# Kernel optimization log

Measured on AMD Instinct MI355X. Metric: run time of the kernel, lower is better.

The kernel has to match this reference:

```python
import jax, jax.numpy as jnp
import numpy as np

E = 256  # embed_dim == input_chn (required by ln_ff broadcast)
B = 256
LAMBDA_INIT = float(0.8 - 0.6 * np.exp(-0.3 * 1.0))  # layer_index = 1


def rmsnorm(x, scale, d, eps=1e-8):
    # matches torch RMSNorm: rms = ||x||_2 / sqrt(d); x / (rms + eps) * scale
    norm = jnp.linalg.norm(x, axis=-1, keepdims=True)
    rms = norm * (d ** -0.5)
    return scale * (x / (rms + eps))


def setup_inputs() -> dict:
    key = jax.random.key(0)
    ks = jax.random.split(key, 12)
    x = jax.random.normal(ks[0], (B, E, E), jnp.float32)
    s = 0.02
    return {
        "x": x,
        "Wq": jax.random.normal(ks[1], (E, 2 * E), jnp.float32) * s,
        "bq": jnp.zeros((2 * E,), jnp.float32),
        "Wk": jax.random.normal(ks[2], (E, 2 * E), jnp.float32) * s,
        "bk": jnp.zeros((2 * E,), jnp.float32),
        "Wv": jax.random.normal(ks[3], (E, E), jnp.float32) * s,
        "bv": jnp.zeros((E,), jnp.float32),
        "lq1": jax.random.normal(ks[4], (E,), jnp.float32) * 0.1,
        "lk1": jax.random.normal(ks[5], (E,), jnp.float32) * 0.1,
        "lq2": jax.random.normal(ks[6], (E,), jnp.float32) * 0.1,
        "lk2": jax.random.normal(ks[7], (E,), jnp.float32) * 0.1,
        "ln_attn_scale": jnp.ones((E,), jnp.float32),
        "norm_scale": jnp.ones((E,), jnp.float32),
        "ln_ff_scale": jnp.ones((E,), jnp.float32),
        "W1": jax.random.normal(ks[8], (E, 4 * E), jnp.float32) * s,
        "b1": jnp.zeros((4 * E,), jnp.float32),
        "W2": jax.random.normal(ks[9], (4 * E, E), jnp.float32) * s,
        "b2": jnp.zeros((E,), jnp.float32),
    }


def reference(x, Wq, bq, Wk, bk, Wv, bv, lq1, lk1, lq2, lk2,
              ln_attn_scale, norm_scale, ln_ff_scale, W1, b1, W2, b2):
    scale = E ** -0.25
    # a = ln_attn(x^T)^T  (normalize over seq dim which equals E)
    a = jnp.swapaxes(rmsnorm(jnp.swapaxes(x, -1, -2), ln_attn_scale, E), -1, -2)
    # decompose: moving average kernel=5, stride=1, edge-replicate padding 2 on seq dim
    ap = jnp.pad(a, ((0, 0), (2, 2), (0, 0)), mode="edge")
    trend = (ap[:, 0:-4] + ap[:, 1:-3] + ap[:, 2:-2] + ap[:, 3:-1] + ap[:, 4:]) / 5.0
    seasonal = a - trend
    # Q from trend, K from seasonal, V from a; all projected along the seq(=E) dim
    q = jnp.swapaxes(trend, -1, -2) @ Wq + bq          # [B, C, 2E]
    q1, q2 = jnp.split(q, 2, axis=-1)
    k = jnp.swapaxes(seasonal, -1, -2) @ Wk + bk       # [B, C, 2E]
    k1, k2 = jnp.split(k, 2, axis=-1)
    v = jnp.swapaxes(a, -1, -2) @ Wv + bv              # [B, C, E]
    a1 = jnp.einsum("bce,bde->bcd", q1, k1) * scale    # [B, C, C]
    a2 = jnp.einsum("bce,bde->bcd", q2, k2) * scale
    lam = jnp.exp(jnp.sum(lq1 * lk1)) - jnp.exp(jnp.sum(lq2 * lk2)) + LAMBDA_INIT
    d = jax.nn.softmax(a1, axis=-1) - lam * jax.nn.softmax(a2, axis=-1)
    attn = rmsnorm(d @ v, norm_scale, E) * (1.0 - LAMBDA_INIT)  # [B, C, E]
    x = x + jnp.swapaxes(attn, -1, -2)
    # FFN branch: ln_ff over last dim (chn == E), then project along seq dim
    h = jnp.swapaxes(rmsnorm(x, ln_ff_scale, E), -1, -2)        # [B, C, E]
    h = jax.nn.silu(h @ W1 + b1) @ W2 + b2                      # [B, C, E]
    x = x + jnp.swapaxes(h, -1, -2)
    return x
```

## Files before the change

### kernel.cpp

```cpp
#include <hip/hip_runtime.h>
#include <math.h>

static constexpr int E = 256;
static constexpr int BTOT = 256;

typedef __bf16 bf16;
typedef __bf16 bf16x8 __attribute__((ext_vector_type(8)));
typedef __bf16 bf16x4 __attribute__((ext_vector_type(4)));
typedef float f32x4 __attribute__((ext_vector_type(4)));

__device__ __forceinline__ void gload16(const void* g, void* l) {
  __builtin_amdgcn_global_load_lds(
      (const __attribute__((address_space(1))) void*)g,
      (__attribute__((address_space(3))) void*)l, 16, 0, 0);
}

__device__ __forceinline__ void xcd_decode(int b, int NX, int nPanels, int& x, int& g) {
  if ((nPanels & 7) == 0) {
    int gLo = b & 7;
    int t2 = b >> 3;
    x = t2 % NX;
    g = (t2 / NX) * 8 + gLo;
  } else {
    x = b % NX;
    g = b / NX;
  }
}

__device__ __forceinline__ float fsig(float x) {
  return __fdividef(1.0f, 1.0f + __expf(-x));
}

__global__ __launch_bounds__(256) void k_wT(const float* __restrict__ src,
                                            bf16* __restrict__ dst, int R, int C) {
  __shared__ float lds[32][33];
  int tiles_c = C >> 5;
  int tc = blockIdx.x % tiles_c;
  int tr = blockIdx.x / tiles_c;
  int r0 = tr << 5, c0 = tc << 5;
  int t = threadIdx.x, cc = t & 31, rr0 = t >> 5;
#pragma unroll
  for (int p = 0; p < 4; ++p) {
    int rr = rr0 + p * 8;
    lds[rr][cc] = src[(size_t)(r0 + rr) * C + (c0 + cc)];
  }
  __syncthreads();
#pragma unroll
  for (int p = 0; p < 4; ++p) {
    int rr = rr0 + p * 8;
    dst[(size_t)(c0 + rr) * R + (r0 + cc)] = (bf16)lds[cc][rr];
  }
}

__global__ void k_lam(const float* lq1, const float* lk1, const float* lq2,
                      const float* lk2, float lambda_init, float* lamOut) {
  int t = threadIdx.x;
  float v1 = lq1[t] * lk1[t];
  float v2 = lq2[t] * lk2[t];
  __shared__ float s1[4], s2[4];
#pragma unroll
  for (int o = 32; o; o >>= 1) { v1 += __shfl_xor(v1, o); v2 += __shfl_xor(v2, o); }
  if ((t & 63) == 0) { s1[t >> 6] = v1; s2[t >> 6] = v2; }
  __syncthreads();
  if (t == 0) {
    float a = s1[0] + s1[1] + s1[2] + s1[3];
    float b = s2[0] + s2[1] + s2[2] + s2[3];
    *lamOut = expf(a) - expf(b) + lambda_init;
  }
}

__global__ __launch_bounds__(1024) void k_rmsA(const float* __restrict__ x, int batchBase,
                                               float* __restrict__ rinvA) {
  __shared__ float red[4][257];
  int lz = blockIdx.x;
  int g = batchBase + lz;
  int t = threadIdx.x, j = t & 255, qd = t >> 8;
  const float* xb = x + (size_t)g * E * E;
  float s = 0.f;
#pragma unroll 4
  for (int ii = 0; ii < 64; ++ii) {
    float v = xb[(size_t)(qd * 64 + ii) * E + j];
    s += v * v;
  }
  red[qd][j] = s;
  __syncthreads();
  if (qd == 0) {
    float tot = red[0][j] + red[1][j] + red[2][j] + red[3][j];
    rinvA[lz * E + j] = __fdividef(1.0f, sqrtf(tot) * 0.0625f + 1e-8f);
  }
}

__global__ __launch_bounds__(256) void k_prep(const float* __restrict__ x, int batchBase,
                                              const float* __restrict__ rinvA,
                                              const float* __restrict__ lnattn,
                                              bf16* __restrict__ a_t,
                                              bf16* __restrict__ tr_t, bf16* __restrict__ se_t) {
  __shared__ float lA[36][261];
  int lz = blockIdx.y, g = batchBase + lz;
  int i0 = blockIdx.x << 5;
  int t = threadIdx.x;
  const float* xb = x + (size_t)g * E * E;
  float rj = rinvA[lz * E + t];
#pragma unroll
  for (int rr = 0; rr < 36; ++rr) {
    int gi = i0 - 2 + rr;
    gi = gi < 0 ? 0 : (gi > 255 ? 255 : gi);
    float v = xb[(size_t)gi * E + t];
    lA[rr][t] = lnattn[gi] * v * rj;
  }
  __syncthreads();
  size_t bo = (size_t)lz * E * E;
  int ic = t & 31, jg = t >> 5;
#pragma unroll 4
  for (int jj = 0; jj < 32; ++jj) {
    int j = jg + jj * 8;
    float a0 = lA[ic][j], a1 = lA[ic + 1][j], a2 = lA[ic + 2][j];
    float a3 = lA[ic + 3][j], a4 = lA[ic + 4][j];
    float tr = (a0 + a1 + a2 + a3 + a4) * 0.2f;
    size_t o = bo + (size_t)j * E + i0 + ic;
    a_t[o] = (bf16)a2;
    tr_t[o] = (bf16)tr;
    se_t[o] = (bf16)(a2 - tr);
  }
}

__global__ __launch_bounds__(256) void gemm_qk(
    const bf16* __restrict__ A1, const bf16* __restrict__ A2,
    const bf16* __restrict__ B1, const bf16* __restrict__ B2,
    bf16* __restrict__ O1, bf16* __restrict__ O2,
    const float* __restrict__ bias1, const float* __restrict__ bias2, int cnt) {
  __shared__ __align__(128) bf16 As[128][64];
  __shared__ __align__(128) bf16 Bs[128][64];
  int xdec, gdec;
  xcd_decode(blockIdx.x, 4, 4 * cnt, xdec, gdec);
  int lz = gdec >> 2;
  int sel = (gdec >> 1) & 1;
  int mb = (gdec & 1) << 7, nb = xdec << 7;
  const bf16* Ab = (sel ? A2 : A1) + (size_t)lz * 65536;
  const bf16* Bb = sel ? B2 : B1;
  bf16* Out = (sel ? O2 : O1) + (size_t)lz * 131072;
  const float* biasN = sel ? bias2 : bias1;
  int t = threadIdx.x, lane = t & 63, wv = t >> 6;
  int wr = wv >> 1, wc = wv & 1;
  int lrow = lane >> 3;
  int kel = ((lane & 7) ^ lrow) << 3;
  f32x4 acc[4][4];
  const f32x4 z4 = {0.f, 0.f, 0.f, 0.f};
#pragma unroll
  for (int a = 0; a < 4; ++a)
#pragma unroll
    for (int b = 0; b < 4; ++b) acc[a][b] = z4;
  for (int k0 = 0; k0 < 256; k0 += 64) {
    __syncthreads();
#pragma unroll
    for (int i = 0; i < 4; ++i) {
      int rb = i * 32 + wv * 8;
      gload16(&Ab[(size_t)(mb + rb + lrow) * 256 + k0 + kel], &As[rb][0]);
      gload16(&Bb[(size_t)(nb + rb + lrow) * 256 + k0 + kel], &Bs[rb][0]);
    }
    __syncthreads();
    __builtin_amdgcn_s_setprio(1);
#pragma unroll
    for (int kk = 0; kk < 2; ++kk) {
      int kb = (kk * 64 + ((lane >> 4) << 4)) ^ ((lane & 7) << 4);
      bf16x8 af[4], bfr[4];
#pragma unroll
      for (int mi = 0; mi < 4; ++mi)
        af[mi] = *(const bf16x8*)((const char*)As + (wr * 64 + mi * 16 + (lane & 15)) * 128 + kb);
#pragma unroll
      for (int ni = 0; ni < 4; ++ni)
        bfr[ni] = *(const bf16x8*)((const char*)Bs + (wc * 64 + ni * 16 + (lane & 15)) * 128 + kb);
#pragma unroll
      for (int mi = 0; mi < 4; ++mi)
#pragma unroll
        for (int ni = 0; ni < 4; ++ni)
          acc[mi][ni] = __builtin_amdgcn_mfma_f32_16x16x32_bf16(af[mi], bfr[ni],
                                                                acc[mi][ni], 0, 0, 0);
    }
    __builtin_amdgcn_s_setprio(0);
  }
  int colB = nb + wc * 64 + (lane & 15);
  int rowB = mb + wr * 64 + ((lane >> 4) << 2);
#pragma unroll
  for (int mi = 0; mi < 4; ++mi) {
#pragma unroll
    for (int ni = 0; ni < 4; ++ni) {
      int col = colB + ni * 16;
      float bN = biasN[col];
#pragma unroll
      for (int r = 0; r < 4; ++r) {
        int row = rowB + mi * 16 + r;
        Out[(size_t)row * 512 + col] = (bf16)(acc[mi][ni][r] + bN);
      }
    }
  }
}

template <int EPI>
__global__ __launch_bounds__(256) void gemm_bt(
    const bf16* __restrict__ A, int lda, size_t aStride,
    const bf16* __restrict__ B, int ldb, size_t bStride,
    bf16* __restrict__ Out, int ldo, size_t oStride, int K,
    const float* __restrict__ biasN, const float* __restrict__ biasM,
    int NX, int NY, int nPanels) {
  __shared__ __align__(128) bf16 As[128][64];
  __shared__ __align__(128) bf16 Bs[128][64];
  int xdec, gdec;
  xcd_decode(blockIdx.x, NX, nPanels, xdec, gdec);
  int lz = gdec / NY;
  int mb = (gdec % NY) << 7, nb = xdec << 7;
  const bf16* Ab = A + (size_t)lz * aStride;
  const bf16* Bb = B + (size_t)lz * bStride;
  int t = threadIdx.x, lane = t & 63, wv = t >> 6;
  int wr = wv >> 1, wc = wv & 1;
  int lrow = lane >> 3;
  int kel = ((lane & 7) ^ lrow) << 3;
  f32x4 acc[4][4];
  const f32x4 z4 = {0.f, 0.f, 0.f, 0.f};
#pragma unroll
  for (int a = 0; a < 4; ++a)
#pragma unroll
    for (int b = 0; b < 4; ++b) acc[a][b] = z4;
  for (int k0 = 0; k0 < K; k0 += 64) {
    __syncthreads();
#pragma unroll
    for (int i = 0; i < 4; ++i) {
      int rb = i * 32 + wv * 8;
      gload16(&Ab[(size_t)(mb + rb + lrow) * lda + k0 + kel], &As[rb][0]);
      gload16(&Bb[(size_t)(nb + rb + lrow) * ldb + k0 + kel], &Bs[rb][0]);
    }
    __syncthreads();
    __builtin_amdgcn_s_setprio(1);
#pragma unroll
    for (int kk = 0; kk < 2; ++kk) {
      int kb = (kk * 64 + ((lane >> 4) << 4)) ^ ((lane & 7) << 4);
      bf16x8 af[4], bfr[4];
#pragma unroll
      for (int mi = 0; mi < 4; ++mi)
        af[mi] = *(const bf16x8*)((const char*)As + (wr * 64 + mi * 16 + (lane & 15)) * 128 + kb);
#pragma unroll
      for (int ni = 0; ni < 4; ++ni)
        bfr[ni] = *(const bf16x8*)((const char*)Bs + (wc * 64 + ni * 16 + (lane & 15)) * 128 + kb);
#pragma unroll
      for (int mi = 0; mi < 4; ++mi)
#pragma unroll
        for (int ni = 0; ni < 4; ++ni)
          acc[mi][ni] = __builtin_amdgcn_mfma_f32_16x16x32_bf16(af[mi], bfr[ni],
                                                                acc[mi][ni], 0, 0, 0);
    }
    __builtin_amdgcn_s_setprio(0);
  }
  int colB = nb + wc * 64 + (lane & 15);
  int rowB = mb + wr * 64 + ((lane >> 4) << 2);
#pragma unroll
  for (int mi = 0; mi < 4; ++mi) {
#pragma unroll
    for (int ni = 0; ni < 4; ++ni) {
      int col = colB + ni * 16;
      float bN = 0.f;
      if constexpr (EPI == 1) bN = biasN[col];
#pragma unroll
      for (int r = 0; r < 4; ++r) {
        int row = rowB + mi * 16 + r;
        float v = acc[mi][ni][r];
        if constexpr (EPI == 1) {
          Out[(size_t)lz * oStride + (size_t)row * ldo + col] = (bf16)(v + bN);
        } else {
          Out[(size_t)lz * oStride + (size_t)row * ldo + col] = (bf16)(v + biasM[row]);
        }
      }
    }
  }
}

__global__ __launch_bounds__(512) void k_score(const bf16* __restrict__ q,
                                               const bf16* __restrict__ km,
                                               const float* __restrict__ lamPtr,
                                               bf16* __restrict__ D, int nPanels) {
  __shared__ __align__(128) bf16 As[128][64];
  __shared__ __align__(128) bf16 Bs[256][64];
  __shared__ float red[4][128];
  int xdec, lz;
  xcd_decode(blockIdx.x, 2, nPanels, xdec, lz);
  int mb = xdec << 7;
  const bf16* qb = q + (size_t)lz * E * 512;
  const bf16* kb = km + (size_t)lz * E * 512;
  int t = threadIdx.x, lane = t & 63, wv = t >> 6;
  int wr = wv >> 2, wc = wv & 3;
  int lrow = lane >> 3;
  int kel = ((lane & 7) ^ lrow) << 3;
  f32x4 acc1[4][4], acc2[4][4];
  const f32x4 z4 = {0.f, 0.f, 0.f, 0.f};
#pragma unroll
  for (int a = 0; a < 4; ++a)
#pragma unroll
    for (int b = 0; b < 4; ++b) { acc1[a][b] = z4; acc2[a][b] = z4; }
#pragma unroll
  for (int mat = 0; mat < 2; ++mat) {
    f32x4(*acc)[4] = mat == 0 ? acc1 : acc2;
    const bf16* qm = qb + mat * 256;
    const bf16* kmm = kb + mat * 256;
    for (int k0 = 0; k0 < 256; k0 += 64) {
      __syncthreads();
#pragma unroll
      for (int i = 0; i < 2; ++i) {
        int rb = i * 64 + wv * 8;
        gload16(&qm[(size_t)(mb + rb + lrow) * 512 + k0 + kel], &As[rb][0]);
      }
#pragma unroll
      for (int i = 0; i < 4; ++i) {
        int rb = i * 64 + wv * 8;
        gload16(&kmm[(size_t)(rb + lrow) * 512 + k0 + kel], &Bs[rb][0]);
      }
      __syncthreads();
      __builtin_amdgcn_s_setprio(1);
#pragma unroll
      for (int kk = 0; kk < 2; ++kk) {
        int kb2 = (kk * 64 + ((lane >> 4) << 4)) ^ ((lane & 7) << 4);
        bf16x8 af[4], bfr[4];
#pragma unroll
        for (int mi = 0; mi < 4; ++mi)
          af[mi] = *(const bf16x8*)((const char*)As + (wr * 64 + mi * 16 + (lane & 15)) * 128 + kb2);
#pragma unroll
        for (int ni = 0; ni < 4; ++ni)
          bfr[ni] = *(const bf16x8*)((const char*)Bs + (wc * 64 + ni * 16 + (lane & 15)) * 128 + kb2);
#pragma unroll
        for (int mi = 0; mi < 4; ++mi)
#pragma unroll
          for (int ni = 0; ni < 4; ++ni)
            acc[mi][ni] = __builtin_amdgcn_mfma_f32_16x16x32_bf16(af[mi], bfr[ni],
                                                                  acc[mi][ni], 0, 0, 0);
      }
      __builtin_amdgcn_s_setprio(0);
    }
  }
  float lam = *lamPtr;
  int rbase = wr * 64 + ((lane >> 4) << 2);
  float inv1[4][4], inv2[4][4];
  __syncthreads();
#pragma unroll
  for (int mat = 0; mat < 2; ++mat) {
    f32x4(*acc)[4] = mat == 0 ? acc1 : acc2;
    float(*inv)[4] = mat == 0 ? inv1 : inv2;
    float tmp[4][4];
#pragma unroll
    for (int mi = 0; mi < 4; ++mi)
#pragma unroll
      for (int r = 0; r < 4; ++r) {
        float m = fmaxf(fmaxf(acc[mi][0][r], acc[mi][1][r]),
                        fmaxf(acc[mi][2][r], acc[mi][3][r]));
        m = fmaxf(m, __shfl_xor(m, 1));
        m = fmaxf(m, __shfl_xor(m, 2));
        m = fmaxf(m, __shfl_xor(m, 4));
        m = fmaxf(m, __shfl_xor(m, 8));
        tmp[mi][r] = m;
      }
    if ((lane & 15) == 0) {
#pragma unroll
      for (int mi = 0; mi < 4; ++mi)
#pragma unroll
        for (int r = 0; r < 4; ++r) red[wc][rbase + mi * 16 + r] = tmp[mi][r];
    }
    __syncthreads();
#pragma unroll
    for (int mi = 0; mi < 4; ++mi)
#pragma unroll
      for (int r = 0; r < 4; ++r) {
        int rw = rbase + mi * 16 + r;
        tmp[mi][r] = fmaxf(fmaxf(red[0][rw], red[1][rw]), fmaxf(red[2][rw], red[3][rw]));
      }
    __syncthreads();
#pragma unroll
    for (int mi = 0; mi < 4; ++mi)
#pragma unroll
      for (int r = 0; r < 4; ++r) {
        float m = tmp[mi][r], s = 0.f;
#pragma unroll
        for (int ni = 0; ni < 4; ++ni) {
          float p = __expf(0.25f * (acc[mi][ni][r] - m));
          acc[mi][ni][r] = p;
          s += p;
        }
        s += __shfl_xor(s, 1);
        s += __shfl_xor(s, 2);
        s += __shfl_xor(s, 4);
        s += __shfl_xor(s, 8);
        tmp[mi][r] = s;
      }
    if ((lane & 15) == 0) {
#pragma unroll
      for (int mi = 0; mi < 4; ++mi)
#pragma unroll
        for (int r = 0; r < 4; ++r) red[wc][rbase + mi * 16 + r] = tmp[mi][r];
    }
    __syncthreads();
#pragma unroll
    for (int mi = 0; mi < 4; ++mi)
#pragma unroll
      for (int r = 0; r < 4; ++r) {
        int rw = rbase + mi * 16 + r;
        inv[mi][r] = __fdividef(1.0f, red[0][rw] + red[1][rw] + red[2][rw] + red[3][rw]);
      }
    __syncthreads();
  }
  size_t Dbase = (size_t)lz * E * E;
#pragma unroll
  for (int mi = 0; mi < 4; ++mi)
#pragma unroll
    for (int ni = 0; ni < 4; ++ni) {
      int col = wc * 64 + ni * 16 + (lane & 15);
#pragma unroll
      for (int r = 0; r < 4; ++r) {
        int row = mb + rbase + mi * 16 + r;
        D[Dbase + (size_t)row * E + col] =
            (bf16)(acc1[mi][ni][r] * inv1[mi][r] - lam * acc2[mi][ni][r] * inv2[mi][r]);
      }
    }
}

__global__ __launch_bounds__(512) void k_pv(const bf16* __restrict__ Dm,
                                            const bf16* __restrict__ vT,
                                            const float* __restrict__ x, int batchBase,
                                            const float* __restrict__ nscale,
                                            float oml, bf16* __restrict__ Y, int nPanels) {
  __shared__ __align__(128) bf16 As[128][64];
  __shared__ __align__(128) bf16 Bs[256][64];
  __shared__ float red[4][128];
  int xdec, lz;
  xcd_decode(blockIdx.x, 2, nPanels, xdec, lz);
  int mb = xdec << 7;
  const bf16* Ab = Dm + (size_t)lz * E * E;
  const bf16* Bb = vT + (size_t)lz * E * E;
  int t = threadIdx.x, lane = t & 63, wv = t >> 6;
  int wr = wv >> 2, wc = wv & 3;
  int lrow = lane >> 3;
  int kel = ((lane & 7) ^ lrow) << 3;
  f32x4 acc[4][4];
  const f32x4 z4 = {0.f, 0.f, 0.f, 0.f};
#pragma unroll
  for (int a = 0; a < 4; ++a)
#pragma unroll
    for (int b = 0; b < 4; ++b) acc[a][b] = z4;
  for (int k0 = 0; k0 < 256; k0 += 64) {
    __syncthreads();
#pragma unroll
    for (int i = 0; i < 2; ++i) {
      int rb = i * 64 + wv * 8;
      gload16(&Ab[(size_t)(mb + rb + lrow) * E + k0 + kel], &As[rb][0]);
    }
#pragma unroll
    for (int i = 0; i < 4; ++i) {
      int rb = i * 64 + wv * 8;
      gload16(&Bb[(size_t)(rb + lrow) * E + k0 + kel], &Bs[rb][0]);
    }
    __syncthreads();
    __builtin_amdgcn_s_setprio(1);
#pragma unroll
    for (int kk = 0; kk < 2; ++kk) {
      int kb2 = (kk * 64 + ((lane >> 4) << 4)) ^ ((lane & 7) << 4);
      bf16x8 af[4], bfr[4];
#pragma unroll
      for (int mi = 0; mi < 4; ++mi)
        af[mi] = *(const bf16x8*)((const char*)As + (wr * 64 + mi * 16 + (lane & 15)) * 128 + kb2);
#pragma unroll
      for (int ni = 0; ni < 4; ++ni)
        bfr[ni] = *(const bf16x8*)((const char*)Bs + (wc * 64 + ni * 16 + (lane & 15)) * 128 + kb2);
#pragma unroll
      for (int mi = 0; mi < 4; ++mi)
#pragma unroll
        for (int ni = 0; ni < 4; ++ni)
          acc[mi][ni] = __builtin_amdgcn_mfma_f32_16x16x32_bf16(af[mi], bfr[ni],
                                                                acc[mi][ni], 0, 0, 0);
    }
    __builtin_amdgcn_s_setprio(0);
  }
  int rbase = wr * 64 + ((lane >> 4) << 2);
  float rowinv[4][4];
#pragma unroll
  for (int mi = 0; mi < 4; ++mi)
#pragma unroll
    for (int r = 0; r < 4; ++r) {
      float s = 0.f;
#pragma unroll
      for (int ni = 0; ni < 4; ++ni) {
        float v = acc[mi][ni][r];
        s += v * v;
      }
      s += __shfl_xor(s, 1);
      s += __shfl_xor(s, 2);
      s += __shfl_xor(s, 4);
      s += __shfl_xor(s, 8);
      rowinv[mi][r] = s;
    }
  if ((lane & 15) == 0) {
#pragma unroll
    for (int mi = 0; mi < 4; ++mi)
#pragma unroll
      for (int r = 0; r < 4; ++r) red[wc][rbase + mi * 16 + r] = rowinv[mi][r];
  }
  __syncthreads();
#pragma unroll
  for (int mi = 0; mi < 4; ++mi)
#pragma unroll
    for (int r = 0; r < 4; ++r) {
      int rw = rbase + mi * 16 + r;
      float tot = red[0][rw] + red[1][rw] + red[2][rw] + red[3][rw];
      rowinv[mi][r] = oml * __fdividef(1.0f, sqrtf(tot) * 0.0625f + 1e-8f);
    }
  size_t bo = (size_t)lz * E * E;
  const float* xb = x + (size_t)(batchBase + lz) * E * E;
#pragma unroll
  for (int mi = 0; mi < 4; ++mi)
#pragma unroll
    for (int ni = 0; ni < 4; ++ni) {
      int col = wc * 64 + ni * 16 + (lane & 15);
      float ns = nscale[col];
      int row0 = mb + rbase + mi * 16;
      f32x4 xv = *(const f32x4*)&xb[(size_t)col * E + row0];
#pragma unroll
      for (int r = 0; r < 4; ++r) {
        size_t o = bo + (size_t)(row0 + r) * E + col;
        Y[o] = (bf16)(xv[r] + ns * acc[mi][ni][r] * rowinv[mi][r]);
      }
    }
}

__global__ __launch_bounds__(256) void k_ffnorm(const bf16* __restrict__ Y,
                                                const float* __restrict__ lnff,
                                                bf16* __restrict__ xn) {
  __shared__ float red[8][33];
  __shared__ float rl[32];
  int lz = blockIdx.y;
  int i0 = blockIdx.x << 5;
  int t = threadIdx.x, ic = t & 31, jg = t >> 5;
  size_t bo = (size_t)lz * E * E;
  float s = 0.f;
#pragma unroll 4
  for (int jj = 0; jj < 32; ++jj) {
    int j = jg + jj * 8;
    float v = (float)Y[bo + (size_t)j * E + i0 + ic];
    s += v * v;
  }
  red[jg][ic] = s;
  __syncthreads();
  if (jg == 0) {
    float tot = 0.f;
#pragma unroll
    for (int g2 = 0; g2 < 8; ++g2) tot += red[g2][ic];
    rl[ic] = __fdividef(1.0f, sqrtf(tot) * 0.0625f + 1e-8f);
  }
  __syncthreads();
  float rinv = rl[ic];
#pragma unroll 4
  for (int jj = 0; jj < 32; ++jj) {
    int j = jg + jj * 8;
    size_t o = bo + (size_t)j * E + i0 + ic;
    xn[o] = (bf16)(lnff[j] * (float)Y[o] * rinv);
  }
}

__global__ __launch_bounds__(1024) void k_ffn(const bf16* __restrict__ xn,
                                              const bf16* __restrict__ W1T,
                                              const bf16* __restrict__ W2T,
                                              const float* __restrict__ b1,
                                              const float* __restrict__ b2,
                                              const bf16* __restrict__ Y,
                                              int batchBase, float* __restrict__ out) {
  __shared__ __align__(128) char arena[131072];
  char* Hb = arena;
  char* xnL = arena + 32768;
  char* S0 = arena + 65536;
  char* S1 = arena + 98304;
  int bid = blockIdx.x;
  int lz = bid >> 2;
  int c0 = (bid & 3) << 6;
  const bf16* xb = xn + (size_t)lz * E * E + (size_t)c0 * E;
  int t = threadIdx.x, lane = t & 63, wv = t >> 6;
  int lrow = lane >> 3;
  int kel = ((lane & 7) ^ lrow) << 3;
  int l15 = lane & 15, l4 = lane >> 4, l7 = lane & 7;
  int wr1 = wv >> 3, wc1 = wv & 7;
  int wr2 = wv >> 1, wc2 = wv & 1;

  float b1v[4][2];
#pragma unroll
  for (int ch = 0; ch < 4; ++ch)
#pragma unroll
    for (int ni = 0; ni < 2; ++ni)
      b1v[ch][ni] = b1[ch * 256 + wc1 * 32 + ni * 16 + l15];

#pragma unroll
  for (int j = 0; j < 2; ++j) {
    int lin = wv * 2 + j;
    int ksub = lin >> 3, rg = (lin & 7) * 8;
    gload16(&xb[(size_t)(rg + lrow) * E + ksub * 64 + kel], xnL + ksub * 8192 + rg * 128);
  }
#pragma unroll
  for (int i = 0; i < 2; ++i) {
    int rb = i * 128 + wv * 8;
    gload16(&W1T[(size_t)(rb + lrow) * 256 + kel], S0 + rb * 128);
  }

  f32x4 acc2[2][2];
  const f32x4 z4 = {0.f, 0.f, 0.f, 0.f};
  acc2[0][0] = z4; acc2[0][1] = z4; acc2[1][0] = z4; acc2[1][1] = z4;
  int cur = 0;

  for (int ch = 0; ch < 4; ++ch) {
    f32x4 acc1[2][2];
    acc1[0][0] = z4; acc1[0][1] = z4; acc1[1][0] = z4; acc1[1][1] = z4;
    for (int k = 0; k < 4; ++k) {
      char* Sn = cur ? S0 : S1;
      if (k < 3) {
#pragma unroll
        for (int i = 0; i < 2; ++i) {
          int rb = i * 128 + wv * 8;
          gload16(&W1T[(size_t)(ch * 256 + rb + lrow) * 256 + (k + 1) * 64 + kel], Sn + rb * 128);
        }
      } else {
#pragma unroll
        for (int i = 0; i < 2; ++i) {
          int rb = i * 128 + wv * 8;
          gload16(&W2T[(size_t)(rb + lrow) * 1024 + ch * 256 + kel], Sn + rb * 128);
        }
      }
      asm volatile("s_waitcnt vmcnt(2)" ::: "memory");
      __builtin_amdgcn_s_barrier();
      char* Sc = cur ? S1 : S0;
#pragma unroll
      for (int kk = 0; kk < 2; ++kk) {
        int kb = (kk * 64 + (l4 << 4)) ^ (l7 << 4);
        bf16x8 af[2], bfr[2];
#pragma unroll
        for (int mi = 0; mi < 2; ++mi)
          af[mi] = *(const bf16x8*)(xnL + k * 8192 + (wr1 * 32 + mi * 16 + l15) * 128 + kb);
#pragma unroll
        for (int ni = 0; ni < 2; ++ni)
          bfr[ni] = *(const bf16x8*)(Sc + (wc1 * 32 + ni * 16 + l15) * 128 + kb);
#pragma unroll
        for (int mi = 0; mi < 2; ++mi)
#pragma unroll
          for (int ni = 0; ni < 2; ++ni)
            acc1[mi][ni] = __builtin_amdgcn_mfma_f32_16x16x32_bf16(af[mi], bfr[ni],
                                                                   acc1[mi][ni], 0, 0, 0);
      }
      __builtin_amdgcn_s_barrier();
      cur ^= 1;
    }
#pragma unroll
    for (int mi = 0; mi < 2; ++mi)
#pragma unroll
      for (int ni = 0; ni < 2; ++ni) {
        int e1 = wc1 * 32 + ni * 16 + l15;
        float bN = b1v[ch][ni];
#pragma unroll
        for (int r = 0; r < 4; ++r) {
          int c = wr1 * 32 + mi * 16 + l4 * 4 + r;
          float u = acc1[mi][ni][r] + bN;
          float h = u * fsig(u);
          int bo2 = c * 512 + ((((e1 >> 3) ^ (c & 7)) << 4) | ((e1 & 7) * 2));
          *(bf16*)(Hb + bo2) = (bf16)h;
        }
      }
    asm volatile("s_waitcnt lgkmcnt(0)" ::: "memory");
    for (int k = 0; k < 4; ++k) {
      char* Sn = cur ? S0 : S1;
      bool isLast = (ch == 3) && (k == 3);
      if (k < 3) {
#pragma unroll
        for (int i = 0; i < 2; ++i) {
          int rb = i * 128 + wv * 8;
          gload16(&W2T[(size_t)(rb + lrow) * 1024 + ch * 256 + (k + 1) * 64 + kel], Sn + rb * 128);
        }
      } else if (ch < 3) {
#pragma unroll
        for (int i = 0; i < 2; ++i) {
          int rb = i * 128 + wv * 8;
          gload16(&W1T[(size_t)((ch + 1) * 256 + rb + lrow) * 256 + kel], Sn + rb * 128);
        }
      }
      if (isLast) asm volatile("s_waitcnt vmcnt(0)" ::: "memory");
      else        asm volatile("s_waitcnt vmcnt(2)" ::: "memory");
      __builtin_amdgcn_s_barrier();
      char* Sc = cur ? S1 : S0;
#pragma unroll
      for (int kk = 0; kk < 2; ++kk) {
        int kb = (kk * 64 + (l4 << 4)) ^ (l7 << 4);
        int kbH = (k * 128 + kk * 64 + (l4 << 4)) ^ (l7 << 4);
        bf16x8 af[2], bfr[2];
#pragma unroll
        for (int mi = 0; mi < 2; ++mi)
          af[mi] = *(const bf16x8*)(Sc + (wr2 * 32 + mi * 16 + l15) * 128 + kb);
#pragma unroll
        for (int ni = 0; ni < 2; ++ni)
          bfr[ni] = *(const bf16x8*)(Hb + (wc2 * 32 + ni * 16 + l15) * 512 + kbH);
#pragma unroll
        for (int mi = 0; mi < 2; ++mi)
#pragma unroll
          for (int ni = 0; ni < 2; ++ni)
            acc2[mi][ni] = __builtin_amdgcn_mfma_f32_16x16x32_bf16(af[mi], bfr[ni],
                                                                   acc2[mi][ni], 0, 0, 0);
      }
      __builtin_amdgcn_s_barrier();
      cur ^= 1;
    }
  }
  const bf16* Yb = Y + (size_t)lz * E * E;
  float* ob = out + (size_t)(batchBase + lz) * E * E;
#pragma unroll
  for (int mi = 0; mi < 2; ++mi) {
    int e2b = wr2 * 32 + mi * 16 + l4 * 4;
    f32x4 bv = *(const f32x4*)&b2[e2b];
#pragma unroll
    for (int ni = 0; ni < 2; ++ni) {
      int c = c0 + wc2 * 32 + ni * 16 + l15;
      bf16x4 yv = *(const bf16x4*)&Yb[(size_t)c * E + e2b];
#pragma unroll
      for (int r = 0; r < 4; ++r)
        ob[(size_t)(e2b + r) * E + c] = acc2[mi][ni][r] + bv[r] + (float)yv[r];
    }
  }
}

extern "C" void kernel_launch(void* const* d_in, const int* in_sizes, int n_in,
                              void* d_out, int out_size, void* d_ws, size_t ws_size,
                              hipStream_t stream) {
  const float* x = (const float*)d_in[0];
  const float* Wq = (const float*)d_in[1];
  const float* bq = (const float*)d_in[2];
  const float* Wk = (const float*)d_in[3];
  const float* bk = (const float*)d_in[4];
  const float* Wv = (const float*)d_in[5];
  const float* bv = (const float*)d_in[6];
  const float* lq1 = (const float*)d_in[7];
  const float* lk1 = (const float*)d_in[8];
  const float* lq2 = (const float*)d_in[9];
  const float* lk2 = (const float*)d_in[10];
  const float* lnattn = (const float*)d_in[11];
  const float* nscale = (const float*)d_in[12];
  const float* lnff = (const float*)d_in[13];
  const float* W1 = (const float*)d_in[14];
  const float* b1 = (const float*)d_in[15];
  const float* W2 = (const float*)d_in[16];
  const float* b2 = (const float*)d_in[17];
  float* out = (float*)d_out;

  char* ws = (char*)d_ws;
  size_t off = 0;
  auto alloc = [&](size_t bytes) {
    size_t o = off;
    off += (bytes + 255) & ~(size_t)255;
    return o;
  };
  size_t oWqT = alloc(512 * 256 * 2);
  size_t oWkT = alloc(512 * 256 * 2);
  size_t oWvT = alloc(256 * 256 * 2);
  size_t oW1T = alloc(1024 * 256 * 2);
  size_t oW2T = alloc(256 * 1024 * 2);
  size_t oLam = alloc(256);
  size_t weightEnd = off;

  const size_t szH = (size_t)E * E * 2;
  const size_t szQ = (size_t)E * 512 * 2;
  const size_t szRi = 1024;
  size_t perBatch = 4 * szH + 2 * szQ + szRi;
  size_t avail = ws_size > weightEnd ? ws_size - weightEnd : 0;
  int NB = (int)(avail / perBatch);
  if (NB > BTOT) NB = BTOT;
  if (NB < 1) NB = 1;

  size_t o = weightEnd;
  auto allocN = [&](size_t bytes) {
    size_t r = o;
    o += bytes * (size_t)NB;
    return r;
  };
  bf16* pA = (bf16*)(ws + allocN(szH));
  bf16* pTr = (bf16*)(ws + allocN(szH));
  bf16* pSe = (bf16*)(ws + allocN(szH));
  bf16* pVT = (bf16*)(ws + allocN(szH));
  size_t oQK = allocN(2 * szQ);
  float* pRiA = (float*)(ws + allocN(szRi));

  bf16* pQ = (bf16*)(ws + oQK);
  bf16* pK = (bf16*)(ws + oQK + (size_t)NB * szQ);
  bf16* pD = pTr;
  bf16* pY = pA;
  bf16* pXn = pSe;

  bf16* pWqT = (bf16*)(ws + oWqT);
  bf16* pWkT = (bf16*)(ws + oWkT);
  bf16* pWvT = (bf16*)(ws + oWvT);
  bf16* pW1T = (bf16*)(ws + oW1T);
  bf16* pW2T = (bf16*)(ws + oW2T);
  float* pLam = (float*)(ws + oLam);

  const float LAMBDA_INIT = 0.8f - 0.6f * expf(-0.3f);
  const float OML = 1.0f - LAMBDA_INIT;

  k_wT<<<dim3((256 / 32) * (512 / 32)), 256, 0, stream>>>(Wq, pWqT, 256, 512);
  k_wT<<<dim3((256 / 32) * (512 / 32)), 256, 0, stream>>>(Wk, pWkT, 256, 512);
  k_wT<<<dim3((256 / 32) * (256 / 32)), 256, 0, stream>>>(Wv, pWvT, 256, 256);
  k_wT<<<dim3((256 / 32) * (1024 / 32)), 256, 0, stream>>>(W1, pW1T, 256, 1024);
  k_wT<<<dim3((1024 / 32) * (256 / 32)), 256, 0, stream>>>(W2, pW2T, 1024, 256);
  k_lam<<<1, 256, 0, stream>>>(lq1, lk1, lq2, lk2, LAMBDA_INIT, pLam);

  for (int base = 0; base < BTOT; base += NB) {
    int cnt = BTOT - base < NB ? BTOT - base : NB;
    k_rmsA<<<dim3(cnt), 1024, 0, stream>>>(x, base, pRiA);
    k_prep<<<dim3(8, cnt), 256, 0, stream>>>(x, base, pRiA, lnattn, pA, pTr, pSe);
    gemm_qk<<<dim3(16 * cnt), 256, 0, stream>>>(pTr, pSe, pWqT, pWkT, pQ, pK, bq, bk, cnt);
    gemm_bt<2><<<dim3(2 * 2 * cnt), 256, 0, stream>>>(pWvT, 256, 0, pA, 256, 65536,
        pVT, 256, 65536, 256, nullptr, bv, 2, 2, 2 * cnt);
    k_score<<<dim3(2 * cnt), 512, 0, stream>>>(pQ, pK, pLam, pD, cnt);
    k_pv<<<dim3(2 * cnt), 512, 0, stream>>>(pD, pVT, x, base, nscale, OML, pY, cnt);
    k_ffnorm<<<dim3(8, cnt), 256, 0, stream>>>(pY, lnff, pXn);
    k_ffn<<<dim3(4 * cnt), 1024, 0, stream>>>(pXn, pW1T, pW2T, b1, b2, pY, base, out);
  }
}
```

Baseline: 495.5 us.

## Fuse score softmax and PV GEMM into one attention kernel via LDS

```diff
diff --git a/kernel.cpp b/kernel.cpp
--- a/kernel.cpp
+++ b/kernel.cpp
@@ -273,13 +273,17 @@
   }
 }
 
-__global__ __launch_bounds__(512) void k_score(const bf16* __restrict__ q,
-                                               const bf16* __restrict__ km,
-                                               const float* __restrict__ lamPtr,
-                                               bf16* __restrict__ D, int nPanels) {
+__global__ __launch_bounds__(512) void k_attn(const bf16* __restrict__ q,
+                                              const bf16* __restrict__ km,
+                                              const bf16* __restrict__ vT,
+                                              const float* __restrict__ x, int batchBase,
+                                              const float* __restrict__ nscale,
+                                              const float* __restrict__ lamPtr, float oml,
+                                              bf16* __restrict__ Y, int nPanels) {
   __shared__ __align__(128) bf16 As[128][64];
   __shared__ __align__(128) bf16 Bs[256][64];
   __shared__ float red[4][128];
+  __shared__ __align__(128) char Pb[65536];
   int xdec, lz;
   xcd_decode(blockIdx.x, 2, nPanels, xdec, lz);
   int mb = xdec << 7;
@@ -289,6 +293,7 @@
   int wr = wv >> 2, wc = wv & 3;
   int lrow = lane >> 3;
   int kel = ((lane & 7) ^ lrow) << 3;
+  int l15 = lane & 15, l4 = lane >> 4;
   f32x4 acc1[4][4], acc2[4][4];
   const f32x4 z4 = {0.f, 0.f, 0.f, 0.f};
 #pragma unroll
@@ -316,14 +321,14 @@
       __builtin_amdgcn_s_setprio(1);
 #pragma unroll
       for (int kk = 0; kk < 2; ++kk) {
-        int kb2 = (kk * 64 + ((lane >> 4) << 4)) ^ ((lane & 7) << 4);
+        int kb2 = (kk * 64 + (l4 << 4)) ^ ((lane & 7) << 4);
         bf16x8 af[4], bfr[4];
 #pragma unroll
         for (int mi = 0; mi < 4; ++mi)
-          af[mi] = *(const bf16x8*)((const char*)As + (wr * 64 + mi * 16 + (lane & 15)) * 128 + kb2);
+          af[mi] = *(const bf16x8*)((const char*)As + (wr * 64 + mi * 16 + l15) * 128 + kb2);
 #pragma unroll
         for (int ni = 0; ni < 4; ++ni)
-          bfr[ni] = *(const bf16x8*)((const char*)Bs + (wc * 64 + ni * 16 + (lane & 15)) * 128 + kb2);
+          bfr[ni] = *(const bf16x8*)((const char*)Bs + (wc * 64 + ni * 16 + l15) * 128 + kb2);
 #pragma unroll
         for (int mi = 0; mi < 4; ++mi)
 #pragma unroll
@@ -335,7 +340,7 @@
     }
   }
   float lam = *lamPtr;
-  int rbase = wr * 64 + ((lane >> 4) << 2);
+  int rbase = wr * 64 + (l4 << 2);
   float inv1[4][4], inv2[4][4];
   __syncthreads();
 #pragma unroll
@@ -355,7 +360,7 @@
         m = fmaxf(m, __shfl_xor(m, 8));
         tmp[mi][r] = m;
       }
-    if ((lane & 15) == 0) {
+    if (l15 == 0) {
 #pragma unroll
       for (int mi = 0; mi < 4; ++mi)
 #pragma unroll
@@ -387,7 +392,7 @@
         s += __shfl_xor(s, 8);
         tmp[mi][r] = s;
       }
-    if ((lane & 15) == 0) {
+    if (l15 == 0) {
 #pragma unroll
       for (int mi = 0; mi < 4; ++mi)
 #pragma unroll
@@ -403,51 +408,27 @@
       }
     __syncthreads();
   }
-  size_t Dbase = (size_t)lz * E * E;
 #pragma unroll
   for (int mi = 0; mi < 4; ++mi)
 #pragma unroll
     for (int ni = 0; ni < 4; ++ni) {
-      int col = wc * 64 + ni * 16 + (lane & 15);
+      int d = wc * 64 + ni * 16 + l15;
 #pragma unroll
       for (int r = 0; r < 4; ++r) {
-        int row = mb + rbase + mi * 16 + r;
-        D[Dbase + (size_t)row * E + col] =
-            (bf16)(acc1[mi][ni][r] * inv1[mi][r] - lam * acc2[mi][ni][r] * inv2[mi][r]);
-      }
-    }
-}
-
-__global__ __launch_bounds__(512) void k_pv(const bf16* __restrict__ Dm,
-                                            const bf16* __restrict__ vT,
-                                            const float* __restrict__ x, int batchBase,
-                                            const float* __restrict__ nscale,
-                                            float oml, bf16* __restrict__ Y, int nPanels) {
-  __shared__ __align__(128) bf16 As[128][64];
-  __shared__ __align__(128) bf16 Bs[256][64];
-  __shared__ float red[4][128];
-  int xdec, lz;
-  xcd_decode(blockIdx.x, 2, nPanels, xdec, lz);
-  int mb = xdec << 7;
-  const bf16* Ab = Dm + (size_t)lz * E * E;
+        int c = rbase + mi * 16 + r;
+        bf16 p = (bf16)(acc1[mi][ni][r] * inv1[mi][r] - lam * acc2[mi][ni][r] * inv2[mi][r]);
+        *(bf16*)(Pb + c * 512 + ((2 * d) ^ ((c & 7) << 4))) = p;
+      }
+    }
+  asm volatile("s_waitcnt lgkmcnt(0)" ::: "memory");
   const bf16* Bb = vT + (size_t)lz * E * E;
-  int t = threadIdx.x, lane = t & 63, wv = t >> 6;
-  int wr = wv >> 2, wc = wv & 3;
-  int lrow = lane >> 3;
-  int kel = ((lane & 7) ^ lrow) << 3;
   f32x4 acc[4][4];
-  const f32x4 z4 = {0.f, 0.f, 0.f, 0.f};
 #pragma unroll
   for (int a = 0; a < 4; ++a)
 #pragma unroll
     for (int b = 0; b < 4; ++b) acc[a][b] = z4;
   for (int k0 = 0; k0 < 256; k0 += 64) {
     __syncthreads();
-#pragma unroll
-    for (int i = 0; i < 2; ++i) {
-      int rb = i * 64 + wv * 8;
-      gload16(&Ab[(size_t)(mb + rb + lrow) * E + k0 + kel], &As[rb][0]);
-    }
 #pragma unroll
     for (int i = 0; i < 4; ++i) {
       int rb = i * 64 + wv * 8;
@@ -457,14 +438,17 @@
     __builtin_amdgcn_s_setprio(1);
 #pragma unroll
     for (int kk = 0; kk < 2; ++kk) {
-      int kb2 = (kk * 64 + ((lane >> 4) << 4)) ^ ((lane & 7) << 4);
+      int kb2 = (kk * 64 + (l4 << 4)) ^ ((lane & 7) << 4);
       bf16x8 af[4], bfr[4];
 #pragma unroll
-      for (int mi = 0; mi < 4; ++mi)
-        af[mi] = *(const bf16x8*)((const char*)As + (wr * 64 + mi * 16 + (lane & 15)) * 128 + kb2);
+      for (int mi = 0; mi < 4; ++mi) {
+        int c = wr * 64 + mi * 16 + l15;
+        int kbP = (k0 * 2 + kk * 64 + (l4 << 4)) ^ ((c & 7) << 4);
+        af[mi] = *(const bf16x8*)(Pb + c * 512 + kbP);
+      }
 #pragma unroll
       for (int ni = 0; ni < 4; ++ni)
-        bfr[ni] = *(const bf16x8*)((const char*)Bs + (wc * 64 + ni * 16 + (lane & 15)) * 128 + kb2);
+        bfr[ni] = *(const bf16x8*)((const char*)Bs + (wc * 64 + ni * 16 + l15) * 128 + kb2);
 #pragma unroll
       for (int mi = 0; mi < 4; ++mi)
 #pragma unroll
@@ -474,7 +458,6 @@
     }
     __builtin_amdgcn_s_setprio(0);
   }
-  int rbase = wr * 64 + ((lane >> 4) << 2);
   float rowinv[4][4];
 #pragma unroll
   for (int mi = 0; mi < 4; ++mi)
@@ -492,7 +475,8 @@
       s += __shfl_xor(s, 8);
       rowinv[mi][r] = s;
     }
-  if ((lane & 15) == 0) {
+  __syncthreads();
+  if (l15 == 0) {
 #pragma unroll
     for (int mi = 0; mi < 4; ++mi)
 #pragma unroll
@@ -513,7 +497,7 @@
   for (int mi = 0; mi < 4; ++mi)
 #pragma unroll
     for (int ni = 0; ni < 4; ++ni) {
-      int col = wc * 64 + ni * 16 + (lane & 15);
+      int col = wc * 64 + ni * 16 + l15;
       float ns = nscale[col];
       int row0 = mb + rbase + mi * 16;
       f32x4 xv = *(const f32x4*)&xb[(size_t)col * E + row0];
@@ -784,7 +768,6 @@
 
   bf16* pQ = (bf16*)(ws + oQK);
   bf16* pK = (bf16*)(ws + oQK + (size_t)NB * szQ);
-  bf16* pD = pTr;
   bf16* pY = pA;
   bf16* pXn = pSe;
 
@@ -812,8 +795,8 @@
     gemm_qk<<<dim3(16 * cnt), 256, 0, stream>>>(pTr, pSe, pWqT, pWkT, pQ, pK, bq, bk, cnt);
     gemm_bt<2><<<dim3(2 * 2 * cnt), 256, 0, stream>>>(pWvT, 256, 0, pA, 256, 65536,
         pVT, 256, 65536, 256, nullptr, bv, 2, 2, 2 * cnt);
-    k_score<<<dim3(2 * cnt), 512, 0, stream>>>(pQ, pK, pLam, pD, cnt);
-    k_pv<<<dim3(2 * cnt), 512, 0, stream>>>(pD, pVT, x, base, nscale, OML, pY, cnt);
+    k_attn<<<dim3(2 * cnt), 512, 0, stream>>>(pQ, pK, pVT, x, base, nscale, pLam,
+                                              OML, pY, cnt);
     k_ffnorm<<<dim3(8, cnt), 256, 0, stream>>>(pY, lnff, pXn);
     k_ffn<<<dim3(4 * cnt), 1024, 0, stream>>>(pXn, pW1T, pW2T, b1, b2, pY, base, out);
   }
```

Result: faster. 485.4 us (-2.0%).
